# Performance work log

Hardware: AMD Instinct MI355X
Metric: run time of the kernel (lower is better)

Reference implementation:

```python
import jax, jax.numpy as jnp
import numpy as np

B, N, H, V = 8192, 12, 512, 256  # batch, n_columns, hidden_size, per-column vocab
LN_EPS = 1e-5


def setup_inputs() -> dict:
    key = jax.random.key(0)
    k0, k1, k2, k3 = jax.random.split(key, 4)
    return {
        "input_embedding": jax.random.normal(k0, (B, H), dtype=jnp.float32),
        "features": jax.random.randint(k1, (B, N), 0, V),  # one categorical id per column
        "emb_tables": jax.random.normal(k2, (N, V, H), dtype=jnp.float32) * 0.02,
        "ln_gamma": jnp.ones((2 * H,), dtype=jnp.float32),
        "ln_beta": jnp.zeros((2 * H,), dtype=jnp.float32),
        "pred_W": jax.random.normal(k3, (N, 2 * H, V), dtype=jnp.float32) * 0.02,
        "pred_b": jnp.zeros((N, V), dtype=jnp.float32),
    }


def reference(input_embedding, features, emb_tables, ln_gamma, ln_beta, pred_W, pred_b):
    n = features.shape[1]
    # per-column embedding lookup: emb[b, n] = emb_tables[n, features[b, n]]  -> [B, N, H]
    emb = emb_tables[jnp.arange(n)[None, :], features]
    # _make_masked_sums: triu(diagonal=1) mask summed over dim 1 == exclusive prefix sum
    # over the column axis: masked_sums[b, j] = sum_{i < j} emb[b, i]
    masked_sums = jnp.cumsum(emb, axis=1) - emb  # [B, N, H]
    ctx = jnp.broadcast_to(input_embedding[:, None, :], emb.shape)  # [B, N, H]
    x = jnp.concatenate([ctx, masked_sums], axis=-1)  # [B, N, 2H]
    # LayerNorm over last dim, then exact (erf) GELU as in torch nn.GELU default
    mu = jnp.mean(x, axis=-1, keepdims=True)
    var = jnp.mean(jnp.square(x - mu), axis=-1, keepdims=True)
    xn = (x - mu) * jax.lax.rsqrt(var + LN_EPS) * ln_gamma + ln_beta
    act = jax.nn.gelu(xn, approximate=False)
    # per-column predictor heads: logits[b, n, :] = act[b, n, :] @ pred_W[n] + pred_b[n]
    logits = jnp.einsum('bnh,nhv->bnv', act, pred_W) + pred_b
    return logits
```

## Files before the change

### kernel.cpp

```cpp
#include <hip/hip_runtime.h>
#include <stdint.h>

#define B_SZ 8192
#define N_F 12
#define H_DIM 512
#define K_DIM 1024
#define V_DIM 256

typedef __attribute__((ext_vector_type(8))) __bf16 bf16x8;
typedef __attribute__((ext_vector_type(4))) float f32x4;

__device__ inline float gelu_f(float x) {
  float t = 1.5957691216057308f * x * (1.0f + 0.044715f * x * x);
  return x / (1.0f + __expf(-t));
}

__device__ inline void gld_lds16(const void* g, void* l) {
  __builtin_amdgcn_global_load_lds(
      (const __attribute__((address_space(1))) void*)g,
      (__attribute__((address_space(3))) void*)l, 16, 0, 0);
}

__global__ __launch_bounds__(256, 8) void k_prep(
    const float* __restrict__ ie, const int* __restrict__ feat,
    const float* __restrict__ tab, const float* __restrict__ gam,
    const float* __restrict__ bet, __bf16* actA,
    float* __restrict__ stats) {
  const int lane = threadIdx.x & 63;
  const int b = blockIdx.x * 4 + (threadIdx.x >> 6);

  const float* cb = ie + (size_t)b * H_DIM + lane * 8;
  float4 c0 = *(const float4*)cb;
  float4 c1 = *(const float4*)(cb + 4);
  float s = c0.x + c0.y + c0.z + c0.w + c1.x + c1.y + c1.z + c1.w;
  float q = c0.x * c0.x + c0.y * c0.y + c0.z * c0.z + c0.w * c0.w +
            c1.x * c1.x + c1.y * c1.y + c1.z * c1.z + c1.w * c1.w;
#pragma unroll
  for (int o = 1; o < 64; o <<= 1) {
    s += __shfl_xor(s, o, 64);
    q += __shfl_xor(q, o, 64);
  }
  const float S1 = s, Q1 = q;

  const float4 g0 = *(const float4*)(gam + H_DIM + lane * 8);
  const float4 g1 = *(const float4*)(gam + H_DIM + lane * 8 + 4);
  const float4 e0 = *(const float4*)(bet + H_DIM + lane * 8);
  const float4 e1 = *(const float4*)(bet + H_DIM + lane * 8 + 4);

  float r[8];
#pragma unroll
  for (int i = 0; i < 8; ++i) r[i] = 0.f;

  const int sw = (lane & ~7) | ((lane & 7) ^ (b & 7));
  __bf16* arow = actA + (size_t)b * N_F * H_DIM + sw * 8;

  for (int n = 0; n < N_F; ++n) {
    s = 0.f; q = 0.f;
#pragma unroll
    for (int i = 0; i < 8; ++i) { s += r[i]; q += r[i] * r[i]; }
#pragma unroll
    for (int o = 1; o < 64; o <<= 1) {
      s += __shfl_xor(s, o, 64);
      q += __shfl_xor(q, o, 64);
    }
    const float mean = (S1 + s) * (1.0f / 1024.0f);
    const float var = (Q1 + q) * (1.0f / 1024.0f) - mean * mean;
    const float rs = rsqrtf(var + 1e-5f);
    if (lane == 0)
      *(float2*)(stats + ((size_t)b * N_F + n) * 2) = make_float2(mean, rs);

    float4 t0, t1;
    const bool have = (n < N_F - 1);
    if (have) {
      const int f = feat[b * N_F + n];
      const float* tr = tab + ((size_t)n * V_DIM + f) * H_DIM + lane * 8;
      t0 = *(const float4*)tr;
      t1 = *(const float4*)(tr + 4);
    }

    bf16x8 pk;
    pk[0] = (__bf16)gelu_f((r[0] - mean) * rs * g0.x + e0.x);
    pk[1] = (__bf16)gelu_f((r[1] - mean) * rs * g0.y + e0.y);
    pk[2] = (__bf16)gelu_f((r[2] - mean) * rs * g0.z + e0.z);
    pk[3] = (__bf16)gelu_f((r[3] - mean) * rs * g0.w + e0.w);
    pk[4] = (__bf16)gelu_f((r[4] - mean) * rs * g1.x + e1.x);
    pk[5] = (__bf16)gelu_f((r[5] - mean) * rs * g1.y + e1.y);
    pk[6] = (__bf16)gelu_f((r[6] - mean) * rs * g1.z + e1.z);
    pk[7] = (__bf16)gelu_f((r[7] - mean) * rs * g1.w + e1.w);
    *(bf16x8*)(arow + (size_t)n * H_DIM) = pk;

    if (have) {
      r[0] += t0.x; r[1] += t0.y; r[2] += t0.z; r[3] += t0.w;
      r[4] += t1.x; r[5] += t1.y; r[6] += t1.z; r[7] += t1.w;
    }
  }
}

__global__ __launch_bounds__(256) void k_wt(const float* __restrict__ W,
                                            __bf16* __restrict__ Wt) {
  __shared__ float tile[32][33];
  const int bid = blockIdx.x;
  const int n = bid >> 8;
  const int rem = bid & 255;
  const int kt = rem >> 3, vt = rem & 7;
  const int tx = threadIdx.x & 31, ty = threadIdx.x >> 5;
  const float* src = W + (size_t)n * K_DIM * V_DIM;
#pragma unroll
  for (int i = 0; i < 4; ++i) {
    const int k = kt * 32 + ty + i * 8;
    tile[ty + i * 8][tx] = src[(size_t)k * V_DIM + vt * 32 + tx];
  }
  __syncthreads();
  __bf16* dst = Wt + (size_t)n * V_DIM * K_DIM;
  const int t = threadIdx.x;
  if (t < 128) {
    const int v_l = t >> 2, c_l = t & 3;
    const int v = vt * 32 + v_l;
    bf16x8 pk;
#pragma unroll
    for (int e = 0; e < 8; ++e) pk[e] = (__bf16)tile[c_l * 8 + e][v_l];
    const int gc = kt * 4 + c_l;
    const int swc = (gc & ~7) | ((gc & 7) ^ (v & 7));
    *(bf16x8*)(dst + (size_t)v * K_DIM + swc * 8) = pk;
  }
}

__global__ __launch_bounds__(512, 2) void k_gemm(
    const float* __restrict__ ie, const __bf16* actA,
    const __bf16* __restrict__ Wt, const float* __restrict__ stats,
    const float* __restrict__ gam, const float* __restrict__ bet,
    const float* __restrict__ bias, float* out) {
  constexpr int BM = 128, BN = 256, BK = 64;
  __shared__ __align__(16) __bf16 As[BM * BK];
  __shared__ __align__(16) __bf16 Ws[BN * BK];

  const int n = blockIdx.y;
  const int b0 = blockIdx.x * BM;
  const int t = threadIdx.x;
  const int lane = t & 63;
  const int w = t >> 6;
  const int wm = w & 1;
  const int wn = w >> 1;
  const int l15 = lane & 15;
  const int lq = lane >> 4;
  const int lr8 = lane >> 3;
  const int lo8 = lane & 7;

  const __bf16* Wtn = Wt + (size_t)n * V_DIM * K_DIM;

  const int pr = t >> 3;
  const int pm = t & 7;
  bf16x8 ctx[16];
  {
#pragma unroll
    for (int h = 0; h < 2; ++h) {
      const int row = b0 + pr + 64 * h;
      const float2 st = *(const float2*)(stats + ((size_t)row * N_F + n) * 2);
      const float mu = st.x, rs = st.y;
      const float* ierow = ie + (size_t)row * H_DIM;
#pragma unroll
      for (int k8 = 0; k8 < 8; ++k8) {
        const int col = k8 * 64 + pm * 8;
        const float4 x0 = *(const float4*)(ierow + col);
        const float4 x1 = *(const float4*)(ierow + col + 4);
        const float4 gg0 = *(const float4*)(gam + col);
        const float4 gg1 = *(const float4*)(gam + col + 4);
        const float4 bb0 = *(const float4*)(bet + col);
        const float4 bb1 = *(const float4*)(bet + col + 4);
        bf16x8 pk;
        pk[0] = (__bf16)gelu_f((x0.x - mu) * rs * gg0.x + bb0.x);
        pk[1] = (__bf16)gelu_f((x0.y - mu) * rs * gg0.y + bb0.y);
        pk[2] = (__bf16)gelu_f((x0.z - mu) * rs * gg0.z + bb0.z);
        pk[3] = (__bf16)gelu_f((x0.w - mu) * rs * gg0.w + bb0.w);
        pk[4] = (__bf16)gelu_f((x1.x - mu) * rs * gg1.x + bb1.x);
        pk[5] = (__bf16)gelu_f((x1.y - mu) * rs * gg1.y + bb1.y);
        pk[6] = (__bf16)gelu_f((x1.z - mu) * rs * gg1.z + bb1.z);
        pk[7] = (__bf16)gelu_f((x1.w - mu) * rs * gg1.w + bb1.w);
        ctx[k8 * 2 + h] = pk;
      }
    }
  }

  const int swo = (pm ^ (pr & 7)) << 3;

  f32x4 acc[4][4];
#pragma unroll
  for (int i = 0; i < 4; ++i)
#pragma unroll
    for (int j = 0; j < 4; ++j) acc[i][j] = (f32x4){0.f, 0.f, 0.f, 0.f};

#pragma unroll
  for (int kt = 0; kt < 16; ++kt) {
    const int k0 = kt * BK;
    __syncthreads();
#pragma unroll
    for (int p = 0; p < 4; ++p) {
      const int v0 = w * 32 + p * 8;
      gld_lds16(Wtn + (size_t)(v0 + lr8) * K_DIM + k0 + lo8 * 8, Ws + v0 * BK);
    }
    if (kt < 8) {
      *(bf16x8*)(As + (pr)*BK + swo) = ctx[kt * 2 + 0];
      *(bf16x8*)(As + (pr + 64) * BK + swo) = ctx[kt * 2 + 1];
    } else {
#pragma unroll
      for (int p = 0; p < 2; ++p) {
        const int r0 = w * 16 + p * 8;
        gld_lds16(actA + ((size_t)(b0 + r0 + lr8) * N_F + n) * H_DIM +
                      (k0 - H_DIM) + lo8 * 8,
                  As + r0 * BK);
      }
    }
    __syncthreads();
#pragma unroll
    for (int ks = 0; ks < 2; ++ks) {
      const int cs = ks * 4 + lq;
      bf16x8 af[4], bb[4];
#pragma unroll
      for (int i = 0; i < 4; ++i) {
        const int row = wm * 64 + i * 16 + l15;
        af[i] = *(const bf16x8*)(As + row * BK + ((cs ^ (row & 7)) << 3));
      }
#pragma unroll
      for (int j = 0; j < 4; ++j) {
        const int row = wn * 64 + j * 16 + l15;
        bb[j] = *(const bf16x8*)(Ws + row * BK + ((cs ^ (row & 7)) << 3));
      }
#pragma unroll
      for (int i = 0; i < 4; ++i)
#pragma unroll
        for (int j = 0; j < 4; ++j)
          acc[i][j] = __builtin_amdgcn_mfma_f32_16x16x32_bf16(af[i], bb[j],
                                                              acc[i][j], 0, 0, 0);
    }
  }

#pragma unroll
  for (int j = 0; j < 4; ++j) {
    const int v = wn * 64 + j * 16 + l15;
    const float bv = bias[n * V_DIM + v];
#pragma unroll
    for (int i = 0; i < 4; ++i) {
      const int rb = wm * 64 + i * 16 + lq * 4;
#pragma unroll
      for (int r = 0; r < 4; ++r) {
        out[((size_t)(b0 + rb + r) * N_F + n) * V_DIM + v] = acc[i][j][r] + bv;
      }
    }
  }
}

extern "C" void kernel_launch(void* const* d_in, const int* in_sizes, int n_in,
                              void* d_out, int out_size, void* d_ws, size_t ws_size,
                              hipStream_t stream) {
  const float* ie = (const float*)d_in[0];
  const int* feat = (const int*)d_in[1];
  const float* tab = (const float*)d_in[2];
  const float* gam = (const float*)d_in[3];
  const float* bet = (const float*)d_in[4];
  const float* predW = (const float*)d_in[5];
  const float* predb = (const float*)d_in[6];
  float* out = (float*)d_out;

  __bf16* actA = (__bf16*)d_out;

  char* ws = (char*)d_ws;
  float* stats = (float*)ws;
  __bf16* Wt = (__bf16*)(ws + 786432);

  hipLaunchKernelGGL(k_prep, dim3(B_SZ / 4), dim3(256), 0, stream, ie, feat,
                     tab, gam, bet, actA, stats);
  hipLaunchKernelGGL(k_wt, dim3(3072), dim3(256), 0, stream, predW, Wt);
  hipLaunchKernelGGL(k_gemm, dim3(B_SZ / 128, N_F), dim3(512), 0, stream, ie,
                     actA, Wt, stats, gam, bet, predb, out);
}
```

Measured before the change: 273.0 us.

## Interleave context LayerNorm+GELU computation with the masked-sum K tiles of the GEMM

The K loop order is reversed so the first eight tiles consume the precomputed masked-sum activations via async global-to-LDS loads. During those same iterations each thread loads and normalizes its slice of the input embedding into registers, and the context tiles are written to LDS in the last eight iterations. This overlaps the LN/GELU prologue and its global loads with MFMA work instead of running it serially before the loop. Register pressure and the schedule stay similar, since ctx is still held in registers.

Measured after the change: 269.3 us. No clear change (-1.3%).

```diff
diff --git a/kernel.cpp b/kernel.cpp
--- a/kernel.cpp
+++ b/kernel.cpp
@@ -150,65 +150,66 @@
 
   const int pr = t >> 3;
   const int pm = t & 7;
+  const float2 st0 = *(const float2*)(stats + ((size_t)(b0 + pr) * N_F + n) * 2);
+  const float2 st1 =
+      *(const float2*)(stats + ((size_t)(b0 + pr + 64) * N_F + n) * 2);
+
+  const int swo = (pm ^ (pr & 7)) << 3;
+
   bf16x8 ctx[16];
-  {
-#pragma unroll
-    for (int h = 0; h < 2; ++h) {
-      const int row = b0 + pr + 64 * h;
-      const float2 st = *(const float2*)(stats + ((size_t)row * N_F + n) * 2);
-      const float mu = st.x, rs = st.y;
-      const float* ierow = ie + (size_t)row * H_DIM;
-#pragma unroll
-      for (int k8 = 0; k8 < 8; ++k8) {
-        const int col = k8 * 64 + pm * 8;
-        const float4 x0 = *(const float4*)(ierow + col);
-        const float4 x1 = *(const float4*)(ierow + col + 4);
+
+  f32x4 acc[4][4];
+#pragma unroll
+  for (int i = 0; i < 4; ++i)
+#pragma unroll
+    for (int j = 0; j < 4; ++j) acc[i][j] = (f32x4){0.f, 0.f, 0.f, 0.f};
+
+#pragma unroll
+  for (int kt = 0; kt < 16; ++kt) {
+    const int k0p = (kt ^ 8) * BK;
+    __syncthreads();
+#pragma unroll
+    for (int p = 0; p < 4; ++p) {
+      const int v0 = w * 32 + p * 8;
+      gld_lds16(Wtn + (size_t)(v0 + lr8) * K_DIM + k0p + lo8 * 8, Ws + v0 * BK);
+    }
+    if (kt < 8) {
+#pragma unroll
+      for (int p = 0; p < 2; ++p) {
+        const int r0 = w * 16 + p * 8;
+        gld_lds16(actA + ((size_t)(b0 + r0 + lr8) * N_F + n) * H_DIM +
+                      (k0p - H_DIM) + lo8 * 8,
+                  As + r0 * BK);
+      }
+      {
+        const int col = kt * 64 + pm * 8;
         const float4 gg0 = *(const float4*)(gam + col);
         const float4 gg1 = *(const float4*)(gam + col + 4);
         const float4 bb0 = *(const float4*)(bet + col);
         const float4 bb1 = *(const float4*)(bet + col + 4);
-        bf16x8 pk;
-        pk[0] = (__bf16)gelu_f((x0.x - mu) * rs * gg0.x + bb0.x);
-        pk[1] = (__bf16)gelu_f((x0.y - mu) * rs * gg0.y + bb0.y);
-        pk[2] = (__bf16)gelu_f((x0.z - mu) * rs * gg0.z + bb0.z);
-        pk[3] = (__bf16)gelu_f((x0.w - mu) * rs * gg0.w + bb0.w);
-        pk[4] = (__bf16)gelu_f((x1.x - mu) * rs * gg1.x + bb1.x);
-        pk[5] = (__bf16)gelu_f((x1.y - mu) * rs * gg1.y + bb1.y);
-        pk[6] = (__bf16)gelu_f((x1.z - mu) * rs * gg1.z + bb1.z);
-        pk[7] = (__bf16)gelu_f((x1.w - mu) * rs * gg1.w + bb1.w);
-        ctx[k8 * 2 + h] = pk;
-      }
-    }
-  }
-
-  const int swo = (pm ^ (pr & 7)) << 3;
-
-  f32x4 acc[4][4];
-#pragma unroll
-  for (int i = 0; i < 4; ++i)
-#pragma unroll
-    for (int j = 0; j < 4; ++j) acc[i][j] = (f32x4){0.f, 0.f, 0.f, 0.f};
-
-#pragma unroll
-  for (int kt = 0; kt < 16; ++kt) {
-    const int k0 = kt * BK;
-    __syncthreads();
-#pragma unroll
-    for (int p = 0; p < 4; ++p) {
-      const int v0 = w * 32 + p * 8;
-      gld_lds16(Wtn + (size_t)(v0 + lr8) * K_DIM + k0 + lo8 * 8, Ws + v0 * BK);
-    }
-    if (kt < 8) {
-      *(bf16x8*)(As + (pr)*BK + swo) = ctx[kt * 2 + 0];
-      *(bf16x8*)(As + (pr + 64) * BK + swo) = ctx[kt * 2 + 1];
+#pragma unroll
+        for (int h = 0; h < 2; ++h) {
+          const int row = b0 + pr + 64 * h;
+          const float mu = h ? st1.x : st0.x;
+          const float rs = h ? st1.y : st0.y;
+          const float* ip = ie + (size_t)row * H_DIM + col;
+          const float4 x0 = *(const float4*)ip;
+          const float4 x1 = *(const float4*)(ip + 4);
+          bf16x8 pk;
+          pk[0] = (__bf16)gelu_f((x0.x - mu) * rs * gg0.x + bb0.x);
+          pk[1] = (__bf16)gelu_f((x0.y - mu) * rs * gg0.y + bb0.y);
+          pk[2] = (__bf16)gelu_f((x0.z - mu) * rs * gg0.z + bb0.z);
+          pk[3] = (__bf16)gelu_f((x0.w - mu) * rs * gg0.w + bb0.w);
+          pk[4] = (__bf16)gelu_f((x1.x - mu) * rs * gg1.x + bb1.x);
+          pk[5] = (__bf16)gelu_f((x1.y - mu) * rs * gg1.y + bb1.y);
+          pk[6] = (__bf16)gelu_f((x1.z - mu) * rs * gg1.z + bb1.z);
+          pk[7] = (__bf16)gelu_f((x1.w - mu) * rs * gg1.w + bb1.w);
+          ctx[kt * 2 + h] = pk;
+        }
+      }
     } else {
-#pragma unroll
-      for (int p = 0; p < 2; ++p) {
-        const int r0 = w * 16 + p * 8;
-        gld_lds16(actA + ((size_t)(b0 + r0 + lr8) * N_F + n) * H_DIM +
-                      (k0 - H_DIM) + lo8 * 8,
-                  As + r0 * BK);
-      }
+      *(bf16x8*)(As + (pr)*BK + swo) = ctx[(kt - 8) * 2 + 0];
+      *(bf16x8*)(As + (pr + 64) * BK + swo) = ctx[(kt - 8) * 2 + 1];
     }
     __syncthreads();
 #pragma unroll
```
